# Optimization experiments

Measured on AMD Instinct MI355X. Metric: run time of the kernel, lower is better.

Reference implementation:

```python
import jax, jax.numpy as jnp
import numpy as np

TOP_K = 2
EPS = 1e-9

def setup_inputs() -> dict:
    key = jax.random.key(0)
    ks = jax.random.split(key, 8)
    B, L, C, F = 64, 512, 3, 300          # batteries, cycles, channels, curve length
    d_model, d_llm, d_ff, E = 512, 4096, 2048, 8
    s = lambda k, sh: jax.random.normal(k, sh, jnp.float32) * 0.02
    return dict(
        cycle_curve_data=jax.random.normal(ks[0], (B, L, C, F), jnp.float32),
        cycle_numbers=jax.random.uniform(ks[1], (B, 1), jnp.float32),
        DKP_embeddings=jax.random.normal(ks[2], (B, d_llm), jnp.float32),
        gate_W1=s(ks[3], (d_llm + 1, d_ff)), gate_b1=jnp.zeros((d_ff,), jnp.float32),
        gate_W2=s(ks[4], (d_ff, E)), gate_b2=jnp.zeros((E,), jnp.float32),
        expert_W=s(ks[5], (E, C * F, d_model)), expert_b=jnp.zeros((E, d_model), jnp.float32),
        gen_W=s(ks[6], (C * F, d_model)), gen_b=jnp.zeros((d_model,), jnp.float32),
    )

def reference(cycle_curve_data, cycle_numbers, DKP_embeddings,
              gate_W1, gate_b1, gate_W2, gate_b2,
              expert_W, expert_b, gen_W, gen_b):
    B, L, C, F = cycle_curve_data.shape
    # router (PatternRouter_two): 2-layer MLP over [DKP embedding ; cycle number]
    g_in = jnp.concatenate([DKP_embeddings, cycle_numbers], axis=-1)   # [B, d_llm+1]
    h = jax.nn.gelu(g_in @ gate_W1 + gate_b1)
    logits = h @ gate_W2 + gate_b2                                     # [B, E]
    # top-k mask on raw logits (as in source), softmax, mask, renormalize
    _, idx = jax.lax.top_k(logits, TOP_K)
    mask = jnp.zeros(logits.shape, bool).at[jnp.arange(B)[:, None], idx].set(True)
    p = jax.nn.softmax(logits, axis=1)
    g = jnp.where(mask, p, 0.0)
    gates = g / (jnp.sum(g, axis=1, keepdims=True) + EPS)              # [B, E]
    # experts: flatten(start_dim=2) then Linear(3*F -> d_model); combine is linear
    # so fold gates into a per-battery weight: sum_e gates[b,e] * W_e
    x = cycle_curve_data.reshape(B, L, C * F)                          # [B, L, 3F]
    Wb = jnp.einsum('be,eid->bid', gates, expert_W)                    # [B, 3F, d]
    bb = gates @ expert_b                                              # [B, d]
    moe_out = jnp.einsum('bli,bid->bld', x, Wb) + bb[:, None, :]       # [B, L, d]
    general = x @ gen_W + gen_b                                        # [B, L, d]
    # source casts the combined MoE output to bf16 before adding
    return general + moe_out.astype(jnp.bfloat16)
```

## Files before the change

### kernel.cpp

```cpp
#include <hip/hip_runtime.h>
#include <hip/hip_bf16.h>
#include <stdint.h>

typedef __attribute__((ext_vector_type(8))) short short8;
typedef __attribute__((ext_vector_type(4))) short short4v;
typedef __attribute__((ext_vector_type(4))) float f32x4;

__device__ inline unsigned short f2bf(float f) {
    union { float f; uint32_t u; } v; v.f = f;
    uint32_t u = v.u;
    uint32_t r = (u + 0x7FFFu + ((u >> 16) & 1u)) >> 16;
    return (unsigned short)r;
}

__device__ inline short4v pk4(float4 a) {
    short4v r;
    r[0] = (short)f2bf(a.x); r[1] = (short)f2bf(a.y);
    r[2] = (short)f2bf(a.z); r[3] = (short)f2bf(a.w);
    return r;
}

__global__ __launch_bounds__(256) void router1(const float* __restrict__ DKP,
                                               const float* __restrict__ W1,
                                               float* __restrict__ part) {
    __shared__ float gin[16 * 256];
    const int t   = threadIdx.x;
    const int lin = blockIdx.x + 16 * blockIdx.y;
    const int jc  = lin & 7;
    const int bg  = (lin >> 3) & 3;
    const int ks  = lin >> 5;
    const int k0  = ks * 256;
    {
        const int b = t >> 4, q = t & 15;
        #pragma unroll
        for (int s = 0; s < 4; ++s)
            *(float4*)(gin + b * 256 + q * 16 + s * 4) =
                *(const float4*)(DKP + (size_t)(bg * 16 + b) * 4096 + k0 + q * 16 + s * 4);
    }
    __syncthreads();
    const int ja = jc * 256 + t;
    float accA[16];
    #pragma unroll
    for (int b = 0; b < 16; ++b) accA[b] = 0.f;
    #pragma unroll 1
    for (int oct = 0; oct < 32; ++oct) {
        const int kk = oct * 8;
        float wa[8];
        #pragma unroll
        for (int i = 0; i < 8; ++i)
            wa[i] = W1[(size_t)(k0 + kk + i) * 2048 + ja];
        #pragma unroll
        for (int b = 0; b < 16; ++b) {
            float4 g0 = *(const float4*)(gin + b * 256 + kk);
            float4 g1 = *(const float4*)(gin + b * 256 + kk + 4);
            accA[b] += g0.x*wa[0] + g0.y*wa[1] + g0.z*wa[2] + g0.w*wa[3]
                     + g1.x*wa[4] + g1.y*wa[5] + g1.z*wa[6] + g1.w*wa[7];
        }
    }
    #pragma unroll 1
    for (int b = 0; b < 16; ++b)
        part[((size_t)(ks * 64 + bg * 16 + b)) * 2048 + ja] = accA[b];
}

__global__ __launch_bounds__(256) void router23(const float* __restrict__ part,
                                                const float* __restrict__ cyc,
                                                const float* __restrict__ W1,
                                                const float* __restrict__ b1,
                                                const float* __restrict__ W2,
                                                const float* __restrict__ b2,
                                                float4* __restrict__ gates) {
    __shared__ float red[256 * 8];
    __shared__ float lg[8];
    const int b = blockIdx.x, t = threadIdx.x;
    float acc[8];
    #pragma unroll
    for (int e = 0; e < 8; ++e) acc[e] = 0.f;
    #pragma unroll 1
    for (int jj = 0; jj < 8; ++jj) {
        const int j = jj * 256 + t;
        float s = 0.f;
        #pragma unroll
        for (int tt = 0; tt < 16; ++tt)
            s += part[((size_t)tt * 64 + b) * 2048 + j];
        s += cyc[b] * W1[(size_t)4096 * 2048 + j] + b1[j];
        const float u  = s + 0.044715f * s * s * s;
        const float th = tanhf(0.7978845608028654f * u);
        const float hv = 0.5f * s * (1.0f + th);
        const float* w = W2 + (size_t)j * 8;
        #pragma unroll
        for (int e = 0; e < 8; ++e) acc[e] += hv * w[e];
    }
    #pragma unroll
    for (int e = 0; e < 8; ++e) red[t * 8 + e] = acc[e];
    __syncthreads();
    if (t < 8) {
        float s = 0.f;
        for (int r = 0; r < 256; ++r) s += red[r * 8 + t];
        lg[t] = s + b2[t];
    }
    __syncthreads();
    if (t == 0) {
        float l[8];
        #pragma unroll
        for (int e = 0; e < 8; ++e) l[e] = lg[e];
        int e0 = 0;
        #pragma unroll
        for (int e = 1; e < 8; ++e) if (l[e] > l[e0]) e0 = e;
        int e1 = (e0 == 0) ? 1 : 0;
        #pragma unroll
        for (int e = 0; e < 8; ++e) if (e != e0 && l[e] > l[e1]) e1 = e;
        const float m = l[e0];
        float p[8], Z = 0.f;
        #pragma unroll
        for (int e = 0; e < 8; ++e) { p[e] = expf(l[e] - m); Z += p[e]; }
        const float pe0 = p[e0] / Z, pe1 = p[e1] / Z;
        const float s2 = pe0 + pe1 + 1e-9f;
        gates[b] = make_float4(__int_as_float(e0), __int_as_float(e1), pe0 / s2, pe1 / s2);
    }
}

__global__ __launch_bounds__(256) void combine_w(const float* __restrict__ genW,
                                                 const float* __restrict__ expW,
                                                 const float4* __restrict__ gates,
                                                 unsigned short* __restrict__ wc) {
    __shared__ float T[9][32 * 36];
    __shared__ float4 gsh[64];
    const int t  = threadIdx.x;
    const int d0 = blockIdx.x * 32;
    const int i0 = blockIdx.y * 32;
    if (t < 64) gsh[t] = gates[t];
    {
        const int il = t >> 3, d4 = (t & 7) * 4;
        const int i = i0 + il;
        const bool valid = (i < 900);
        const size_t off = (size_t)i * 512 + d0 + d4;
        #pragma unroll
        for (int s = 0; s < 9; ++s) {
            const float* src = (s == 0) ? genW : (expW + (size_t)(s - 1) * 900 * 512);
            float4 v = valid ? *(const float4*)(src + off) : make_float4(0, 0, 0, 0);
            float* Td = &T[s][0];
            Td[(d4 + 0) * 36 + il] = v.x;
            Td[(d4 + 1) * 36 + il] = v.y;
            Td[(d4 + 2) * 36 + il] = v.z;
            Td[(d4 + 3) * 36 + il] = v.w;
        }
    }
    __syncthreads();
    const int dl = t >> 3, sg = t & 7;
    const int fo = dl * 36 + sg * 4;
    unsigned short* wrow = wc + (size_t)(d0 + dl) * 928 + i0 + sg * 4;
    #pragma unroll 1
    for (int b = 0; b < 64; ++b) {
        const float4 gt = gsh[b];
        const int e0 = __float_as_int(gt.x), e1 = __float_as_int(gt.y);
        const float g0 = gt.z, g1 = gt.w;
        float4 G = *(const float4*)&T[0][fo];
        float4 X = *(const float4*)&T[1 + e0][fo];
        float4 Y = *(const float4*)&T[1 + e1][fo];
        short4v r;
        r[0] = (short)f2bf(G.x + g0 * X.x + g1 * Y.x);
        r[1] = (short)f2bf(G.y + g0 * X.y + g1 * Y.y);
        r[2] = (short)f2bf(G.z + g0 * X.z + g1 * Y.z);
        r[3] = (short)f2bf(G.w + g0 * X.w + g1 * Y.w);
        *(short4v*)(wrow + (size_t)b * 512 * 928) = r;
    }
}

__global__ __launch_bounds__(512, 4) void moe_gemm(const float* __restrict__ x,
                                                   const unsigned short* __restrict__ wc,
                                                   const float4* __restrict__ gates,
                                                   const float* __restrict__ eb,
                                                   const float* __restrict__ genb,
                                                   float* __restrict__ out) {
    __shared__ unsigned short As[2][64 * 40];
    __shared__ unsigned short Bs[2][512 * 32];
    const int b  = blockIdx.x;
    const int m0 = blockIdx.y * 64;
    const int t = threadIdx.x, lane = t & 63, wid = t >> 6;
    const float4 gt = gates[b];
    const int e0 = __float_as_int(gt.x), e1 = __float_as_int(gt.y);
    const float g0 = gt.z, g1 = gt.w;
    const float* xb = x + (size_t)b * 512 * 900;
    const unsigned short* wcb = wc + (size_t)b * 512 * 928;
    f32x4 acc[4][4];
    #pragma unroll
    for (int mi = 0; mi < 4; ++mi)
        #pragma unroll
        for (int ni = 0; ni < 4; ++ni)
            acc[mi][ni] = (f32x4){0.f, 0.f, 0.f, 0.f};

    const int arow  = t >> 3;
    const int akoff = (t & 7) * 4;
    const float* xrow = xb + (size_t)(m0 + arow) * 900 + akoff;
    const int bseg = (lane & 3) ^ ((lane >> 3) & 3);
    const int burow = lane >> 2;

    const int wn = wid * 64;
    const int lm = lane & 15, lq = lane >> 4;

    auto loadA = [&](int kt) -> float4 {
        if (kt < 28) return *(const float4*)(xrow + kt * 32);
        float4 z = make_float4(0.f, 0.f, 0.f, 0.f);
        if (akoff == 0) z = *(const float4*)(xrow + 896);
        return z;
    };
    auto stageB = [&](int buf, int kt) {
        const int k0 = kt * 32;
        #pragma unroll
        for (int r = 0; r < 4; ++r) {
            const int chunk = wid * 4 + r;
            const int n = chunk * 16 + burow;
            const unsigned short* gsrc = wcb + (size_t)n * 928 + k0 + bseg * 8;
            unsigned short* ldst = &Bs[buf][chunk * 512];
            __builtin_amdgcn_global_load_lds(
                (const __attribute__((address_space(1))) unsigned int*)gsrc,
                (__attribute__((address_space(3))) unsigned int*)ldst, 16, 0, 0);
        }
    };
    auto packA = [&](int buf, float4 f) {
        *(short4v*)&As[buf][arow * 40 + akoff] = pk4(f);
    };
    auto compute = [&](int buf) {
        short8 af[4], bfr[4];
        #pragma unroll
        for (int mi = 0; mi < 4; ++mi)
            af[mi] = *(const short8*)&As[buf][(mi * 16 + lm) * 40 + lq * 8];
        #pragma unroll
        for (int ni = 0; ni < 4; ++ni) {
            const int n = wn + ni * 16 + lm;
            const int slot = lq ^ ((lm >> 1) & 3);
            bfr[ni] = *(const short8*)&Bs[buf][n * 32 + slot * 8];
        }
        #pragma unroll
        for (int mi = 0; mi < 4; ++mi)
            #pragma unroll
            for (int ni = 0; ni < 4; ++ni)
                acc[mi][ni] = __builtin_amdgcn_mfma_f32_16x16x32_bf16(
                    af[mi], bfr[ni], acc[mi][ni], 0, 0, 0);
    };

#define BAR_V1() do { \
    asm volatile("s_waitcnt vmcnt(1) lgkmcnt(0)\n\ts_barrier" ::: "memory"); \
    __builtin_amdgcn_sched_barrier(0); } while (0)
#define BAR_V0() do { \
    asm volatile("s_waitcnt vmcnt(0) lgkmcnt(0)\n\ts_barrier" ::: "memory"); \
    __builtin_amdgcn_sched_barrier(0); } while (0)

    stageB(0, 0);
    __builtin_amdgcn_sched_barrier(0);
    float4 a_cur  = loadA(0);
    float4 a_next = loadA(1);
    packA(0, a_cur);
    BAR_V1();

    #pragma unroll 1
    for (int p = 0; p < 13; ++p) {
        {
            stageB(1, 2 * p + 1);
            __builtin_amdgcn_sched_barrier(0);
            float4 a2 = loadA(2 * p + 2);
            __builtin_amdgcn_sched_barrier(0);
            compute(0);
            packA(1, a_next);
            a_next = a2;
            BAR_V1();
        }
        {
            stageB(0, 2 * p + 2);
            __builtin_amdgcn_sched_barrier(0);
            float4 a2 = loadA(2 * p + 3);
            __builtin_amdgcn_sched_barrier(0);
            compute(1);
            packA(0, a_next);
            a_next = a2;
            BAR_V1();
        }
    }
    {
        stageB(1, 27);
        __builtin_amdgcn_sched_barrier(0);
        float4 a2 = loadA(28);
        __builtin_amdgcn_sched_barrier(0);
        compute(0);
        packA(1, a_next);
        a_next = a2;
        BAR_V1();
    }
    {
        stageB(0, 28);
        __builtin_amdgcn_sched_barrier(0);
        compute(1);
        packA(0, a_next);
        BAR_V0();
    }
    compute(0);

#undef BAR_V1
#undef BAR_V0

    #pragma unroll
    for (int ni = 0; ni < 4; ++ni) {
        const int col = wn + ni * 16 + lm;
        const float bias = genb[col] + g0 * eb[e0 * 512 + col] + g1 * eb[e1 * 512 + col];
        #pragma unroll
        for (int mi = 0; mi < 4; ++mi) {
            const int row = m0 + mi * 16 + lq * 4;
            #pragma unroll
            for (int r = 0; r < 4; ++r)
                out[((size_t)b * 512 + row + r) * 512 + col] = acc[mi][ni][r] + bias;
        }
    }
}

extern "C" void kernel_launch(void* const* d_in, const int* in_sizes, int n_in,
                              void* d_out, int out_size, void* d_ws, size_t ws_size,
                              hipStream_t stream) {
    const float* x    = (const float*)d_in[0];
    const float* cyc  = (const float*)d_in[1];
    const float* dkp  = (const float*)d_in[2];
    const float* gW1  = (const float*)d_in[3];
    const float* gb1  = (const float*)d_in[4];
    const float* gW2  = (const float*)d_in[5];
    const float* gb2  = (const float*)d_in[6];
    const float* eW   = (const float*)d_in[7];
    const float* eb   = (const float*)d_in[8];
    const float* genW = (const float*)d_in[9];
    const float* genb = (const float*)d_in[10];
    float* out = (float*)d_out;

    char* ws = (char*)d_ws;
    unsigned short* wcomb = (unsigned short*)ws;
    float* part  = (float*)ws;
    float4* gts  = (float4*)(ws + 60817408);

    router1<<<dim3(16, 32), 256, 0, stream>>>(dkp, gW1, part);
    router23<<<64, 256, 0, stream>>>(part, cyc, gW1, gb1, gW2, gb2, gts);
    combine_w<<<dim3(16, 29), 256, 0, stream>>>(genW, eW, gts, wcomb);
    moe_gemm<<<dim3(64, 8), 512, 0, stream>>>(x, wcomb, gts, eb, genb, out);
}
```

Measured before the change: 363.5 us.

## Deepen GEMM B pipeline to four stages, split router reduction, widen combine stores

The MoE GEMM now keeps four LDS buffers for B tiles (prefetch depth three) and remaps the grid so neighbouring blocks share batteries. The intent is to hide global load latency and improve L2 reuse, at the cost of more LDS and lower occupancy. The second router stage is split into a 64x8 grid plus a tiny top-k kernel to add parallelism, which costs one extra launch. router1 software-prefetches W1 rows. combine_w writes 8 bf16 values per store instead of 4.

```diff
diff --git a/kernel.cpp b/kernel.cpp
--- a/kernel.cpp
+++ b/kernel.cpp
@@ -42,81 +42,87 @@
     float accA[16];
     #pragma unroll
     for (int b = 0; b < 16; ++b) accA[b] = 0.f;
-    #pragma unroll 1
+    float wcur[8], wnxt[8];
+    #pragma unroll
+    for (int i = 0; i < 8; ++i)
+        wcur[i] = W1[(size_t)(k0 + i) * 2048 + ja];
+    #pragma unroll 2
     for (int oct = 0; oct < 32; ++oct) {
         const int kk = oct * 8;
-        float wa[8];
-        #pragma unroll
-        for (int i = 0; i < 8; ++i)
-            wa[i] = W1[(size_t)(k0 + kk + i) * 2048 + ja];
+        if (oct < 31) {
+            #pragma unroll
+            for (int i = 0; i < 8; ++i)
+                wnxt[i] = W1[(size_t)(k0 + kk + 8 + i) * 2048 + ja];
+        }
         #pragma unroll
         for (int b = 0; b < 16; ++b) {
             float4 g0 = *(const float4*)(gin + b * 256 + kk);
             float4 g1 = *(const float4*)(gin + b * 256 + kk + 4);
-            accA[b] += g0.x*wa[0] + g0.y*wa[1] + g0.z*wa[2] + g0.w*wa[3]
-                     + g1.x*wa[4] + g1.y*wa[5] + g1.z*wa[6] + g1.w*wa[7];
-        }
+            accA[b] += g0.x*wcur[0] + g0.y*wcur[1] + g0.z*wcur[2] + g0.w*wcur[3]
+                     + g1.x*wcur[4] + g1.y*wcur[5] + g1.z*wcur[6] + g1.w*wcur[7];
+        }
+        #pragma unroll
+        for (int i = 0; i < 8; ++i) wcur[i] = wnxt[i];
     }
     #pragma unroll 1
     for (int b = 0; b < 16; ++b)
         part[((size_t)(ks * 64 + bg * 16 + b)) * 2048 + ja] = accA[b];
 }
 
-__global__ __launch_bounds__(256) void router23(const float* __restrict__ part,
+__global__ __launch_bounds__(256) void router2p(const float* __restrict__ part,
                                                 const float* __restrict__ cyc,
                                                 const float* __restrict__ W1,
                                                 const float* __restrict__ b1,
                                                 const float* __restrict__ W2,
-                                                const float* __restrict__ b2,
-                                                float4* __restrict__ gates) {
+                                                float* __restrict__ plog) {
     __shared__ float red[256 * 8];
-    __shared__ float lg[8];
-    const int b = blockIdx.x, t = threadIdx.x;
-    float acc[8];
-    #pragma unroll
-    for (int e = 0; e < 8; ++e) acc[e] = 0.f;
-    #pragma unroll 1
-    for (int jj = 0; jj < 8; ++jj) {
-        const int j = jj * 256 + t;
-        float s = 0.f;
-        #pragma unroll
-        for (int tt = 0; tt < 16; ++tt)
-            s += part[((size_t)tt * 64 + b) * 2048 + j];
-        s += cyc[b] * W1[(size_t)4096 * 2048 + j] + b1[j];
-        const float u  = s + 0.044715f * s * s * s;
-        const float th = tanhf(0.7978845608028654f * u);
-        const float hv = 0.5f * s * (1.0f + th);
-        const float* w = W2 + (size_t)j * 8;
-        #pragma unroll
-        for (int e = 0; e < 8; ++e) acc[e] += hv * w[e];
-    }
-    #pragma unroll
-    for (int e = 0; e < 8; ++e) red[t * 8 + e] = acc[e];
+    const int b = blockIdx.x, jc = blockIdx.y;
+    const int t = threadIdx.x;
+    const int j = jc * 256 + t;
+    float s = 0.f;
+    #pragma unroll
+    for (int tt = 0; tt < 16; ++tt)
+        s += part[((size_t)tt * 64 + b) * 2048 + j];
+    s += cyc[b] * W1[(size_t)4096 * 2048 + j] + b1[j];
+    const float u  = s + 0.044715f * s * s * s;
+    const float th = tanhf(0.7978845608028654f * u);
+    const float hv = 0.5f * s * (1.0f + th);
+    const float* w = W2 + (size_t)j * 8;
+    #pragma unroll
+    for (int e = 0; e < 8; ++e) red[t * 8 + e] = hv * w[e];
     __syncthreads();
     if (t < 8) {
-        float s = 0.f;
-        for (int r = 0; r < 256; ++r) s += red[r * 8 + t];
-        lg[t] = s + b2[t];
-    }
-    __syncthreads();
-    if (t == 0) {
-        float l[8];
-        #pragma unroll
-        for (int e = 0; e < 8; ++e) l[e] = lg[e];
-        int e0 = 0;
-        #pragma unroll
-        for (int e = 1; e < 8; ++e) if (l[e] > l[e0]) e0 = e;
-        int e1 = (e0 == 0) ? 1 : 0;
-        #pragma unroll
-        for (int e = 0; e < 8; ++e) if (e != e0 && l[e] > l[e1]) e1 = e;
-        const float m = l[e0];
-        float p[8], Z = 0.f;
-        #pragma unroll
-        for (int e = 0; e < 8; ++e) { p[e] = expf(l[e] - m); Z += p[e]; }
-        const float pe0 = p[e0] / Z, pe1 = p[e1] / Z;
-        const float s2 = pe0 + pe1 + 1e-9f;
-        gates[b] = make_float4(__int_as_float(e0), __int_as_float(e1), pe0 / s2, pe1 / s2);
-    }
+        float acc = 0.f;
+        for (int r = 0; r < 256; ++r) acc += red[r * 8 + t];
+        plog[((size_t)b * 8 + jc) * 8 + t] = acc;
+    }
+}
+
+__global__ __launch_bounds__(64) void router4(const float* __restrict__ plog,
+                                              const float* __restrict__ b2,
+                                              float4* __restrict__ gates) {
+    const int b = threadIdx.x;
+    float l[8];
+    #pragma unroll
+    for (int e = 0; e < 8; ++e) l[e] = b2[e];
+    #pragma unroll
+    for (int jc = 0; jc < 8; ++jc)
+        #pragma unroll
+        for (int e = 0; e < 8; ++e)
+            l[e] += plog[((size_t)b * 8 + jc) * 8 + e];
+    int e0 = 0;
+    #pragma unroll
+    for (int e = 1; e < 8; ++e) if (l[e] > l[e0]) e0 = e;
+    int e1 = (e0 == 0) ? 1 : 0;
+    #pragma unroll
+    for (int e = 0; e < 8; ++e) if (e != e0 && l[e] > l[e1]) e1 = e;
+    const float m = l[e0];
+    float p[8], Z = 0.f;
+    #pragma unroll
+    for (int e = 0; e < 8; ++e) { p[e] = expf(l[e] - m); Z += p[e]; }
+    const float pe0 = p[e0] / Z, pe1 = p[e1] / Z;
+    const float s2 = pe0 + pe1 + 1e-9f;
+    gates[b] = make_float4(__int_as_float(e0), __int_as_float(e1), pe0 / s2, pe1 / s2);
 }
 
 __global__ __launch_bounds__(256) void combine_w(const float* __restrict__ genW,
@@ -146,36 +152,44 @@
         }
     }
     __syncthreads();
-    const int dl = t >> 3, sg = t & 7;
-    const int fo = dl * 36 + sg * 4;
-    unsigned short* wrow = wc + (size_t)(d0 + dl) * 928 + i0 + sg * 4;
-    #pragma unroll 1
-    for (int b = 0; b < 64; ++b) {
+    const int bb = t >> 7;
+    const int dl = (t >> 2) & 31;
+    const int sg = t & 3;
+    const int fo = dl * 36 + sg * 8;
+    unsigned short* wrow = wc + (size_t)(d0 + dl) * 928 + i0 + sg * 8;
+    #pragma unroll 2
+    for (int bp = 0; bp < 32; ++bp) {
+        const int b = bp * 2 + bb;
         const float4 gt = gsh[b];
         const int e0 = __float_as_int(gt.x), e1 = __float_as_int(gt.y);
         const float g0 = gt.z, g1 = gt.w;
-        float4 G = *(const float4*)&T[0][fo];
-        float4 X = *(const float4*)&T[1 + e0][fo];
-        float4 Y = *(const float4*)&T[1 + e1][fo];
-        short4v r;
-        r[0] = (short)f2bf(G.x + g0 * X.x + g1 * Y.x);
-        r[1] = (short)f2bf(G.y + g0 * X.y + g1 * Y.y);
-        r[2] = (short)f2bf(G.z + g0 * X.z + g1 * Y.z);
-        r[3] = (short)f2bf(G.w + g0 * X.w + g1 * Y.w);
-        *(short4v*)(wrow + (size_t)b * 512 * 928) = r;
-    }
-}
-
-__global__ __launch_bounds__(512, 4) void moe_gemm(const float* __restrict__ x,
-                                                   const unsigned short* __restrict__ wc,
-                                                   const float4* __restrict__ gates,
-                                                   const float* __restrict__ eb,
-                                                   const float* __restrict__ genb,
-                                                   float* __restrict__ out) {
+        float4 Ga = *(const float4*)&T[0][fo],      Gb = *(const float4*)&T[0][fo + 4];
+        float4 Xa = *(const float4*)&T[1 + e0][fo], Xb = *(const float4*)&T[1 + e0][fo + 4];
+        float4 Ya = *(const float4*)&T[1 + e1][fo], Yb = *(const float4*)&T[1 + e1][fo + 4];
+        short8 r;
+        r[0] = (short)f2bf(Ga.x + g0 * Xa.x + g1 * Ya.x);
+        r[1] = (short)f2bf(Ga.y + g0 * Xa.y + g1 * Ya.y);
+        r[2] = (short)f2bf(Ga.z + g0 * Xa.z + g1 * Ya.z);
+        r[3] = (short)f2bf(Ga.w + g0 * Xa.w + g1 * Ya.w);
+        r[4] = (short)f2bf(Gb.x + g0 * Xb.x + g1 * Yb.x);
+        r[5] = (short)f2bf(Gb.y + g0 * Xb.y + g1 * Yb.y);
+        r[6] = (short)f2bf(Gb.z + g0 * Xb.z + g1 * Yb.z);
+        r[7] = (short)f2bf(Gb.w + g0 * Xb.w + g1 * Yb.w);
+        *(short8*)(wrow + (size_t)b * 512 * 928) = r;
+    }
+}
+
+__global__ __launch_bounds__(512) void moe_gemm(const float* __restrict__ x,
+                                                const unsigned short* __restrict__ wc,
+                                                const float4* __restrict__ gates,
+                                                const float* __restrict__ eb,
+                                                const float* __restrict__ genb,
+                                                float* __restrict__ out) {
     __shared__ unsigned short As[2][64 * 40];
-    __shared__ unsigned short Bs[2][512 * 32];
-    const int b  = blockIdx.x;
-    const int m0 = blockIdx.y * 64;
+    __shared__ unsigned short Bs[4][512 * 32];
+    const int g  = blockIdx.x;
+    const int b  = (g & 7) + 8 * (g >> 6);
+    const int m0 = ((g >> 3) & 7) * 64;
     const int t = threadIdx.x, lane = t & 63, wid = t >> 6;
     const float4 gt = gates[b];
     const int e0 = __float_as_int(gt.x), e1 = __float_as_int(gt.y);
@@ -200,9 +214,10 @@
 
     auto loadA = [&](int kt) -> float4 {
         if (kt < 28) return *(const float4*)(xrow + kt * 32);
-        float4 z = make_float4(0.f, 0.f, 0.f, 0.f);
-        if (akoff == 0) z = *(const float4*)(xrow + 896);
-        return z;
+        const float* p = xrow + 896 - (akoff ? 32 : 0);
+        float4 raw = *(const float4*)p;
+        if (akoff) raw = make_float4(0.f, 0.f, 0.f, 0.f);
+        return raw;
     };
     auto stageB = [&](int buf, int kt) {
         const int k0 = kt * 32;
@@ -224,7 +239,7 @@
         short8 af[4], bfr[4];
         #pragma unroll
         for (int mi = 0; mi < 4; ++mi)
-            af[mi] = *(const short8*)&As[buf][(mi * 16 + lm) * 40 + lq * 8];
+            af[mi] = *(const short8*)&As[buf & 1][(mi * 16 + lm) * 40 + lq * 8];
         #pragma unroll
         for (int ni = 0; ni < 4; ++ni) {
             const int n = wn + ni * 16 + lm;
@@ -239,64 +254,33 @@
                     af[mi], bfr[ni], acc[mi][ni], 0, 0, 0);
     };
 
-#define BAR_V1() do { \
-    asm volatile("s_waitcnt vmcnt(1) lgkmcnt(0)\n\ts_barrier" ::: "memory"); \
-    __builtin_amdgcn_sched_barrier(0); } while (0)
-#define BAR_V0() do { \
-    asm volatile("s_waitcnt vmcnt(0) lgkmcnt(0)\n\ts_barrier" ::: "memory"); \
-    __builtin_amdgcn_sched_barrier(0); } while (0)
-
-    stageB(0, 0);
-    __builtin_amdgcn_sched_barrier(0);
-    float4 a_cur  = loadA(0);
-    float4 a_next = loadA(1);
-    packA(0, a_cur);
-    BAR_V1();
-
+#define BARN(n) asm volatile("s_waitcnt vmcnt(" #n ") lgkmcnt(0)\n\ts_barrier" ::: "memory")
+
+    float4 a_next;
+    {
+        float4 a0 = loadA(0);
+        stageB(0, 0);
+        a_next = loadA(1);
+        stageB(1, 1);
+        stageB(2, 2);
+        packA(0, a0);
+        BARN(9);
+    }
     #pragma unroll 1
-    for (int p = 0; p < 13; ++p) {
-        {
-            stageB(1, 2 * p + 1);
-            __builtin_amdgcn_sched_barrier(0);
-            float4 a2 = loadA(2 * p + 2);
-            __builtin_amdgcn_sched_barrier(0);
-            compute(0);
-            packA(1, a_next);
-            a_next = a2;
-            BAR_V1();
-        }
-        {
-            stageB(0, 2 * p + 2);
-            __builtin_amdgcn_sched_barrier(0);
-            float4 a2 = loadA(2 * p + 3);
-            __builtin_amdgcn_sched_barrier(0);
-            compute(1);
-            packA(0, a_next);
-            a_next = a2;
-            BAR_V1();
-        }
-    }
-    {
-        stageB(1, 27);
-        __builtin_amdgcn_sched_barrier(0);
-        float4 a2 = loadA(28);
-        __builtin_amdgcn_sched_barrier(0);
-        compute(0);
-        packA(1, a_next);
-        a_next = a2;
-        BAR_V1();
-    }
-    {
-        stageB(0, 28);
-        __builtin_amdgcn_sched_barrier(0);
-        compute(1);
-        packA(0, a_next);
-        BAR_V0();
-    }
+    for (int q = 0; q < 6; ++q) {
+        const int tb = q * 4;
+        { float4 a2 = loadA(tb + 2); stageB(3, tb + 3); compute(0); packA(1, a_next); a_next = a2; BARN(9); }
+        { float4 a2 = loadA(tb + 3); stageB(0, tb + 4); compute(1); packA(0, a_next); a_next = a2; BARN(9); }
+        { float4 a2 = loadA(tb + 4); stageB(1, tb + 5); compute(2); packA(1, a_next); a_next = a2; BARN(9); }
+        { float4 a2 = loadA(tb + 5); stageB(2, tb + 6); compute(3); packA(0, a_next); a_next = a2; BARN(9); }
+    }
+    { float4 a2 = loadA(26); stageB(3, 27); compute(0); packA(1, a_next); a_next = a2; BARN(9); }
+    { float4 a2 = loadA(27); stageB(0, 28); compute(1); packA(0, a_next); a_next = a2; BARN(9); }
+    { float4 a2 = loadA(28); compute(2); packA(1, a_next); a_next = a2; BARN(5); }
+    { compute(3); packA(0, a_next); BARN(0); }
     compute(0);
 
-#undef BAR_V1
-#undef BAR_V0
+#undef BARN
 
     #pragma unroll
     for (int ni = 0; ni < 4; ++ni) {
@@ -332,9 +316,11 @@
     unsigned short* wcomb = (unsigned short*)ws;
     float* part  = (float*)ws;
     float4* gts  = (float4*)(ws + 60817408);
+    float* plog  = (float*)(ws + 60817408 + 1024);
 
     router1<<<dim3(16, 32), 256, 0, stream>>>(dkp, gW1, part);
-    router23<<<64, 256, 0, stream>>>(part, cyc, gW1, gb1, gW2, gb2, gts);
+    router2p<<<dim3(64, 8), 256, 0, stream>>>(part, cyc, gW1, gb1, gW2, plog);
+    router4<<<1, 64, 0, stream>>>(plog, gb2, gts);
     combine_w<<<dim3(16, 29), 256, 0, stream>>>(genW, eW, gts, wcomb);
-    moe_gemm<<<dim3(64, 8), 512, 0, stream>>>(x, wcomb, gts, eb, genb, out);
-}
+    moe_gemm<<<512, 512, 0, stream>>>(x, wcomb, gts, eb, genb, out);
+}
```

After: 335.2 us. 1.08x faster.
